# Optimization experiments

Measured on AMD Instinct MI355X. Metric: run time of the kernel, lower is better.

## Reference

```python
import jax, jax.numpy as jnp
import numpy as np


def setup_inputs() -> dict:
    key = jax.random.key(0)
    k1, k2, k3, k4 = jax.random.split(key, 4)
    B, S, d_in, d_out = 4, 2048, 1024, 1024
    x = jax.random.normal(k1, (B, S, d_in), dtype=jnp.float32)
    # torch nn.Linear weight is [d_out, d_in]; we store transposed [d_in, d_out]
    Wq = jax.random.normal(k2, (d_in, d_out), dtype=jnp.float32) * (1.0 / np.sqrt(d_in))
    Wk = jax.random.normal(k3, (d_in, d_out), dtype=jnp.float32) * (1.0 / np.sqrt(d_in))
    Wv = jax.random.normal(k4, (d_in, d_out), dtype=jnp.float32) * (1.0 / np.sqrt(d_in))
    return {"x": x, "Wq": Wq, "Wk": Wk, "Wv": Wv}


def reference(x, Wq, Wk, Wv):
    # x: [B, S, d_in]
    B, S, d_in = x.shape
    q = jnp.einsum("bsd,de->bse", x, Wq)
    k = jnp.einsum("bsd,de->bse", x, Wk)
    v = jnp.einsum("bsd,de->bse", x, Wv)
    scores = jnp.einsum("bqe,bke->bqk", q, k)  # [B, S, S]
    causal = jnp.triu(jnp.ones((S, S), dtype=bool), k=1)  # True above diagonal
    scores = jnp.where(causal[None, :, :], -jnp.inf, scores)
    # NOTE: original scales by sqrt(d_in), not sqrt(d_out)
    scale = jnp.asarray(1.0 / np.sqrt(d_in), dtype=scores.dtype)
    weights = jax.nn.softmax(scores * scale, axis=-1)
    # dropout p=0.0 -> identity
    return jnp.einsum("bqk,bke->bqe", weights, v)
```

## Files before the change

kernel.cpp:

```cpp
#include <hip/hip_runtime.h>
#include <hip/hip_bf16.h>

typedef __attribute__((ext_vector_type(8))) short short8;
typedef __attribute__((ext_vector_type(4))) float f32x4;
typedef unsigned short ushort_t;

__device__ __forceinline__ ushort_t f2bf(float f) {
    union { __hip_bfloat16 h; ushort_t u; } c;
    c.h = __float2bfloat16(f);
    return c.u;
}

__device__ __forceinline__ void gload16(const ushort_t* g, ushort_t* l) {
    __builtin_amdgcn_global_load_lds(
        (const __attribute__((address_space(1))) void*)g,
        (__attribute__((address_space(3))) void*)l, 16, 0, 0);
}

__global__ __launch_bounds__(256) void k_convert_x(const float* __restrict__ x,
                                                   ushort_t* __restrict__ xb) {
    size_t idx = ((size_t)blockIdx.x * 256 + threadIdx.x) * 8;
    float4 a = *(const float4*)(x + idx);
    float4 b = *(const float4*)(x + idx + 4);
    short8 o;
    o[0] = (short)f2bf(a.x); o[1] = (short)f2bf(a.y);
    o[2] = (short)f2bf(a.z); o[3] = (short)f2bf(a.w);
    o[4] = (short)f2bf(b.x); o[5] = (short)f2bf(b.y);
    o[6] = (short)f2bf(b.z); o[7] = (short)f2bf(b.w);
    *(short8*)(xb + idx) = o;
}

__global__ __launch_bounds__(256) void k_transpose_w(const float* __restrict__ W0,
                                                     const float* __restrict__ W1,
                                                     const float* __restrict__ W2,
                                                     ushort_t* __restrict__ Wt) {
    const float* W = (blockIdx.z == 0) ? W0 : (blockIdx.z == 1) ? W1 : W2;
    ushort_t* out = Wt + (size_t)blockIdx.z * 1024 * 1024;
    __shared__ float tile[32][33];
    int tx = threadIdx.x, ty = threadIdx.y;
    int d0 = blockIdx.y * 32, e0 = blockIdx.x * 32;
#pragma unroll
    for (int i = 0; i < 32; i += 8)
        tile[ty + i][tx] = W[(size_t)(d0 + ty + i) * 1024 + e0 + tx];
    __syncthreads();
#pragma unroll
    for (int i = 0; i < 32; i += 8)
        out[(size_t)(e0 + ty + i) * 1024 + d0 + tx] = f2bf(tile[tx][ty + i]);
}

__global__ __launch_bounds__(256) void k_transpose_v(const ushort_t* __restrict__ V,
                                                     ushort_t* __restrict__ Vt) {
    int b = blockIdx.z;
    const ushort_t* in = V + (size_t)b * 2048 * 1024;
    ushort_t* out = Vt + (size_t)b * 1024 * 2048;
    __shared__ ushort_t tile[32][33];
    int tx = threadIdx.x, ty = threadIdx.y;
    int e0 = blockIdx.x * 32, j0 = blockIdx.y * 32;
#pragma unroll
    for (int i = 0; i < 32; i += 8)
        tile[ty + i][tx] = in[(size_t)(j0 + ty + i) * 1024 + e0 + tx];
    __syncthreads();
#pragma unroll
    for (int i = 0; i < 32; i += 8)
        out[(size_t)(e0 + ty + i) * 2048 + j0 + tx] = tile[tx][ty + i];
}

template <int MODE>
__global__ __launch_bounds__(256) void k_gemm(const ushort_t* __restrict__ Abase,
                                              const ushort_t* __restrict__ Bbase,
                                              void* __restrict__ Cbase) {
    const int bz = blockIdx.z;
    int bm, bn;
    const ushort_t* A;
    const ushort_t* B;
    int lda, ldb, nk;
    if constexpr (MODE == 0) {
        bm = blockIdx.x; bn = blockIdx.y;
        A = Abase; lda = 1024;
        B = Bbase + (size_t)bz * 1024 * 1024; ldb = 1024;
        nk = 32;
    } else if constexpr (MODE == 1) {
        int x = blockIdx.x;
        bm = (int)((sqrtf(8.f * x + 1.f) - 1.f) * 0.5f);
        while ((bm + 1) * (bm + 2) / 2 <= x) ++bm;
        while (bm * (bm + 1) / 2 > x) --bm;
        bn = x - bm * (bm + 1) / 2;
        A = Abase + (size_t)bz * 2048 * 1024; lda = 1024;
        B = Bbase + (size_t)bz * 2048 * 1024; ldb = 1024;
        nk = 32;
    } else {
        int xr = blockIdx.x;
        bm = (xr & 1) ? (15 - (xr >> 1)) : (xr >> 1);
        bn = blockIdx.y;
        A = Abase + (size_t)bz * 2048 * 2048; lda = 2048;
        B = Bbase + (size_t)bz * 1024 * 2048; ldb = 2048;
        nk = (bm + 1) * 4;
    }

    __shared__ ushort_t As[128 * 32];
    __shared__ ushort_t Bs[128 * 32];

    const int tid = threadIdx.x;
    const int l = tid & 63, wid = tid >> 6;
    const int wr = (wid >> 1) * 64, wc = (wid & 1) * 64;
    const int lr = l & 15, kc = (l >> 4) * 8;

    const int srow = tid >> 2, skb = (tid & 3) * 8;
    const ushort_t* ag = A + (size_t)(bm * 128 + srow) * lda + skb;
    const ushort_t* bg = B + (size_t)(bn * 128 + srow) * ldb + skb;
    const size_t a64 = (size_t)64 * lda, b64 = (size_t)64 * ldb;
    ushort_t* al = As + tid * 8;
    ushort_t* bl = Bs + tid * 8;

    f32x4 zero = {0.f, 0.f, 0.f, 0.f};
    f32x4 acc[4][4];
#pragma unroll
    for (int m = 0; m < 4; ++m)
#pragma unroll
        for (int n = 0; n < 4; ++n) acc[m][n] = zero;

    f32x4 rs[4];
    short8 ones;
#pragma unroll
    for (int e = 0; e < 8; ++e) ones[e] = (short)0x3F80;
#pragma unroll
    for (int m = 0; m < 4; ++m) rs[m] = zero;

    for (int ks = 0; ks < nk; ++ks) {
        __syncthreads();
        gload16(ag, al);
        gload16(ag + a64, al + 2048);
        gload16(bg, bl);
        gload16(bg + b64, bl + 2048);
        ag += 32; bg += 32;
        __syncthreads();

        short8 a[4], b[4];
#pragma unroll
        for (int m = 0; m < 4; ++m)
            a[m] = *(const short8*)&As[(wr + m * 16 + lr) * 32 + kc];
#pragma unroll
        for (int n = 0; n < 4; ++n)
            b[n] = *(const short8*)&Bs[(wc + n * 16 + lr) * 32 + kc];
#pragma unroll
        for (int m = 0; m < 4; ++m)
#pragma unroll
            for (int n = 0; n < 4; ++n)
                acc[m][n] = __builtin_amdgcn_mfma_f32_16x16x32_bf16(a[m], b[n], acc[m][n], 0, 0, 0);
        if constexpr (MODE == 2) {
#pragma unroll
            for (int m = 0; m < 4; ++m)
                rs[m] = __builtin_amdgcn_mfma_f32_16x16x32_bf16(a[m], ones, rs[m], 0, 0, 0);
        }
    }

    const int rbase = (l >> 4) * 4;
    const int cbase = l & 15;

    float inv[4][4];
    if constexpr (MODE == 2) {
#pragma unroll
        for (int m = 0; m < 4; ++m)
#pragma unroll
            for (int r = 0; r < 4; ++r) inv[m][r] = 1.0f / rs[m][r];
    }

#pragma unroll
    for (int m = 0; m < 4; ++m) {
#pragma unroll
        for (int n = 0; n < 4; ++n) {
            int row0 = wr + m * 16 + rbase;
            int col = wc + n * 16 + cbase;
            int gcol = bn * 128 + col;
#pragma unroll
            for (int r = 0; r < 4; ++r) {
                int grow = bm * 128 + row0 + r;
                float v = acc[m][n][r];
                if constexpr (MODE == 0) {
                    ushort_t* C = (ushort_t*)Cbase + (size_t)bz * 8192 * 1024;
                    C[(size_t)grow * 1024 + gcol] = f2bf(v);
                } else if constexpr (MODE == 1) {
                    ushort_t* C = (ushort_t*)Cbase + (size_t)bz * 2048 * 2048;
                    ushort_t pv = (gcol <= grow) ? f2bf(__expf(v * 0.03125f))
                                                 : (ushort_t)0;
                    C[(size_t)grow * 2048 + gcol] = pv;
                } else {
                    float* C = (float*)Cbase + (size_t)bz * 2048 * 1024;
                    C[(size_t)grow * 1024 + gcol] = v * inv[m][r];
                }
            }
        }
    }
}

extern "C" void kernel_launch(void* const* d_in, const int* in_sizes, int n_in,
                              void* d_out, int out_size, void* d_ws, size_t ws_size,
                              hipStream_t stream) {
    const float* x  = (const float*)d_in[0];
    const float* Wq = (const float*)d_in[1];
    const float* Wk = (const float*)d_in[2];
    const float* Wv = (const float*)d_in[3];

    char* ws = (char*)d_ws;
    ushort_t* xb     = (ushort_t*)(ws);
    ushort_t* Wt     = (ushort_t*)(ws + 16777216);
    ushort_t* QKV    = (ushort_t*)(ws + 23068672);
    ushort_t* Vt     = (ushort_t*)(ws + 73400320);
    ushort_t* P      = (ushort_t*)(ws + 90177536);

    ushort_t* Q = QKV;
    ushort_t* K = QKV + (size_t)8192 * 1024;
    ushort_t* V = QKV + (size_t)2 * 8192 * 1024;

    k_convert_x<<<4096, 256, 0, stream>>>(x, xb);
    k_transpose_w<<<dim3(32, 32, 3), dim3(32, 8), 0, stream>>>(Wq, Wk, Wv, Wt);
    k_gemm<0><<<dim3(64, 8, 3), 256, 0, stream>>>(xb, Wt, QKV);
    k_transpose_v<<<dim3(32, 64, 4), dim3(32, 8), 0, stream>>>(V, Vt);
    k_gemm<1><<<dim3(136, 1, 4), 256, 0, stream>>>(Q, K, P);
    k_gemm<2><<<dim3(16, 8, 4), 256, 0, stream>>>(P, Vt, (float*)d_out);
}
```

Before: 181.2 us.

## Fuse V transpose into QKV GEMM epilogue and merge prep kernels

The x conversion and the weight transposes now run in a single prep kernel, and the separate V transpose kernel is gone. The V slice of the QKV GEMM writes its tile transposed through padded shared memory straight into Vt. This removes two launches and a full round trip of V through global memory. In exchange, the MODE 0 GEMM uses more shared memory (which can lower occupancy), and the V blocks run a longer epilogue with extra synchronisation.

```diff
diff --git a/kernel.cpp b/kernel.cpp
--- a/kernel.cpp
+++ b/kernel.cpp
@@ -17,25 +17,32 @@
         (__attribute__((address_space(3))) void*)l, 16, 0, 0);
 }
 
-__global__ __launch_bounds__(256) void k_convert_x(const float* __restrict__ x,
-                                                   ushort_t* __restrict__ xb) {
-    size_t idx = ((size_t)blockIdx.x * 256 + threadIdx.x) * 8;
-    float4 a = *(const float4*)(x + idx);
-    float4 b = *(const float4*)(x + idx + 4);
-    short8 o;
-    o[0] = (short)f2bf(a.x); o[1] = (short)f2bf(a.y);
-    o[2] = (short)f2bf(a.z); o[3] = (short)f2bf(a.w);
-    o[4] = (short)f2bf(b.x); o[5] = (short)f2bf(b.y);
-    o[6] = (short)f2bf(b.z); o[7] = (short)f2bf(b.w);
-    *(short8*)(xb + idx) = o;
-}
-
-__global__ __launch_bounds__(256) void k_transpose_w(const float* __restrict__ W0,
-                                                     const float* __restrict__ W1,
-                                                     const float* __restrict__ W2,
-                                                     ushort_t* __restrict__ Wt) {
-    const float* W = (blockIdx.z == 0) ? W0 : (blockIdx.z == 1) ? W1 : W2;
-    ushort_t* out = Wt + (size_t)blockIdx.z * 1024 * 1024;
+__global__ __launch_bounds__(256) void k_prep(const float* __restrict__ x,
+                                              const float* __restrict__ W0,
+                                              const float* __restrict__ W1,
+                                              const float* __restrict__ W2,
+                                              ushort_t* __restrict__ xb,
+                                              ushort_t* __restrict__ Wt) {
+    const int bz = blockIdx.z;
+    if (bz == 3) {
+        const int t = threadIdx.y * 32 + threadIdx.x;
+        size_t base = ((size_t)(blockIdx.y * 32 + blockIdx.x) * 256 + t) * 8;
+#pragma unroll
+        for (int p = 0; p < 4; ++p) {
+            size_t idx = base + (size_t)p * 2097152;
+            float4 a = *(const float4*)(x + idx);
+            float4 b = *(const float4*)(x + idx + 4);
+            short8 o;
+            o[0] = (short)f2bf(a.x); o[1] = (short)f2bf(a.y);
+            o[2] = (short)f2bf(a.z); o[3] = (short)f2bf(a.w);
+            o[4] = (short)f2bf(b.x); o[5] = (short)f2bf(b.y);
+            o[6] = (short)f2bf(b.z); o[7] = (short)f2bf(b.w);
+            *(short8*)(xb + idx) = o;
+        }
+        return;
+    }
+    const float* W = (bz == 0) ? W0 : (bz == 1) ? W1 : W2;
+    ushort_t* out = Wt + (size_t)bz * 1024 * 1024;
     __shared__ float tile[32][33];
     int tx = threadIdx.x, ty = threadIdx.y;
     int d0 = blockIdx.y * 32, e0 = blockIdx.x * 32;
@@ -48,27 +55,11 @@
         out[(size_t)(e0 + ty + i) * 1024 + d0 + tx] = f2bf(tile[tx][ty + i]);
 }
 
-__global__ __launch_bounds__(256) void k_transpose_v(const ushort_t* __restrict__ V,
-                                                     ushort_t* __restrict__ Vt) {
-    int b = blockIdx.z;
-    const ushort_t* in = V + (size_t)b * 2048 * 1024;
-    ushort_t* out = Vt + (size_t)b * 1024 * 2048;
-    __shared__ ushort_t tile[32][33];
-    int tx = threadIdx.x, ty = threadIdx.y;
-    int e0 = blockIdx.x * 32, j0 = blockIdx.y * 32;
-#pragma unroll
-    for (int i = 0; i < 32; i += 8)
-        tile[ty + i][tx] = in[(size_t)(j0 + ty + i) * 1024 + e0 + tx];
-    __syncthreads();
-#pragma unroll
-    for (int i = 0; i < 32; i += 8)
-        out[(size_t)(e0 + ty + i) * 2048 + j0 + tx] = tile[tx][ty + i];
-}
-
 template <int MODE>
 __global__ __launch_bounds__(256) void k_gemm(const ushort_t* __restrict__ Abase,
                                               const ushort_t* __restrict__ Bbase,
-                                              void* __restrict__ Cbase) {
+                                              void* __restrict__ Cbase,
+                                              ushort_t* __restrict__ Vt) {
     const int bz = blockIdx.z;
     int bm, bn;
     const ushort_t* A;
@@ -97,8 +88,10 @@
         nk = (bm + 1) * 4;
     }
 
-    __shared__ ushort_t As[128 * 32];
-    __shared__ ushort_t Bs[128 * 32];
+    constexpr int SMEM_ELEMS = (MODE == 0) ? (128 * 130) : 8192;
+    __shared__ ushort_t smem[SMEM_ELEMS];
+    ushort_t* As = smem;
+    ushort_t* Bs = smem + 4096;
 
     const int tid = threadIdx.x;
     const int l = tid & 63, wid = tid >> 6;
@@ -156,6 +149,32 @@
 
     const int rbase = (l >> 4) * 4;
     const int cbase = l & 15;
+
+    if constexpr (MODE == 0) {
+        if (bz == 2) {
+            __syncthreads();
+#pragma unroll
+            for (int m = 0; m < 4; ++m)
+#pragma unroll
+                for (int n = 0; n < 4; ++n) {
+                    int col = wc + n * 16 + cbase;
+                    int row0 = wr + m * 16 + rbase;
+#pragma unroll
+                    for (int r = 0; r < 4; ++r)
+                        smem[col * 130 + row0 + r] = f2bf(acc[m][n][r]);
+                }
+            __syncthreads();
+            const int e = tid >> 1, jh = (tid & 1) * 64;
+            const int b = bm >> 4, j0 = (bm * 128) & 2047;
+            ushort_t* dst = Vt + (size_t)b * 2097152 +
+                            (size_t)(bn * 128 + e) * 2048 + j0 + jh;
+            const ushort_t* src = smem + e * 130 + jh;
+#pragma unroll
+            for (int c = 0; c < 8; ++c)
+                *(short8*)(dst + c * 8) = *(const short8*)(src + c * 8);
+            return;
+        }
+    }
 
     float inv[4][4];
     if constexpr (MODE == 2) {
@@ -210,12 +229,9 @@
 
     ushort_t* Q = QKV;
     ushort_t* K = QKV + (size_t)8192 * 1024;
-    ushort_t* V = QKV + (size_t)2 * 8192 * 1024;
-
-    k_convert_x<<<4096, 256, 0, stream>>>(x, xb);
-    k_transpose_w<<<dim3(32, 32, 3), dim3(32, 8), 0, stream>>>(Wq, Wk, Wv, Wt);
-    k_gemm<0><<<dim3(64, 8, 3), 256, 0, stream>>>(xb, Wt, QKV);
-    k_transpose_v<<<dim3(32, 64, 4), dim3(32, 8), 0, stream>>>(V, Vt);
-    k_gemm<1><<<dim3(136, 1, 4), 256, 0, stream>>>(Q, K, P);
-    k_gemm<2><<<dim3(16, 8, 4), 256, 0, stream>>>(P, Vt, (float*)d_out);
-}
+
+    k_prep<<<dim3(32, 32, 4), dim3(32, 8), 0, stream>>>(x, Wq, Wk, Wv, xb, Wt);
+    k_gemm<0><<<dim3(64, 8, 3), 256, 0, stream>>>(xb, Wt, QKV, Vt);
+    k_gemm<1><<<dim3(136, 1, 4), 256, 0, stream>>>(Q, K, P, nullptr);
+    k_gemm<2><<<dim3(16, 8, 4), 256, 0, stream>>>(P, Vt, (float*)d_out, nullptr);
+}
```

Measured after the change: 173.9 us. -4.0%, faster.
